# Kernel tuning notes

Hardware: AMD Instinct MI355X
Metric: run time of the kernel (lower is better)

Reference implementation:

```python
import jax, jax.numpy as jnp
import numpy as np

CHUNK = 256  # points per lax.map step; keeps [CHUNK, F] intermediates small


def _point_tri_sqdist(p_chunk, a, b, c):
    """Squared distance from each point to each triangle (Ericson closest-point).
    p_chunk: [C,3]; a,b,c: [F,3] -> returns [C,F]."""
    p = p_chunk[:, None, :]          # [C,1,3]
    a = a[None]; b = b[None]; c = c[None]  # [1,F,3]
    ab = b - a
    ac = c - a
    ap = p - a
    d1 = jnp.sum(ab * ap, -1)
    d2 = jnp.sum(ac * ap, -1)
    bp = p - b
    d3 = jnp.sum(ab * bp, -1)
    d4 = jnp.sum(ac * bp, -1)
    cp = p - c
    d5 = jnp.sum(ab * cp, -1)
    d6 = jnp.sum(ac * cp, -1)
    vc_ = d1 * d4 - d3 * d2
    vb_ = d5 * d2 - d1 * d6
    va_ = d3 * d6 - d5 * d4
    # safe-guarded edge / interior parameters
    den_ab = d1 - d3
    v_ab = d1 / jnp.where(den_ab != 0, den_ab, 1.0)
    den_ac = d2 - d6
    w_ac = d2 / jnp.where(den_ac != 0, den_ac, 1.0)
    den_bc = (d4 - d3) + (d5 - d6)
    w_bc = (d4 - d3) / jnp.where(den_bc != 0, den_bc, 1.0)
    den_in = va_ + vb_ + vc_
    inv = 1.0 / jnp.where(den_in != 0, den_in, 1.0)
    v_in = vb_ * inv
    w_in = vc_ * inv
    # candidate closest point; later writes take priority (vertex regions last)
    q = a + ab * v_in[..., None] + ac * w_in[..., None]                      # interior
    q = jnp.where(((va_ <= 0) & (d4 - d3 >= 0) & (d5 - d6 >= 0))[..., None],
                  b + (c - b) * w_bc[..., None], q)                          # edge bc
    q = jnp.where(((vb_ <= 0) & (d2 >= 0) & (d6 <= 0))[..., None],
                  a + ac * w_ac[..., None], q)                               # edge ac
    q = jnp.where(((vc_ <= 0) & (d1 >= 0) & (d3 <= 0))[..., None],
                  a + ab * v_ab[..., None], q)                               # edge ab
    q = jnp.where(((d6 >= 0) & (d5 <= d6))[..., None], c, q)                 # vertex c
    q = jnp.where(((d3 >= 0) & (d4 <= d3))[..., None], b, q)                 # vertex b
    q = jnp.where(((d1 <= 0) & (d2 <= 0))[..., None], a, q)                  # vertex a
    return jnp.sum((p - q) ** 2, -1)


def _mesh_sdf(verts, faces, points):
    va = verts[faces[:, 0]]
    vb = verts[faces[:, 1]]
    vc = verts[faces[:, 2]]

    def per_chunk(pc):
        d = _point_tri_sqdist(pc, va, vb, vc)   # [CHUNK, F]
        return jnp.min(d, axis=-1), jnp.argmin(d, axis=-1)

    P = points.shape[0]
    dists, assoc = jax.lax.map(per_chunk, points.reshape(P // CHUNK, CHUNK, 3))
    dist = dists.reshape(P)
    assoc = assoc.reshape(P).astype(jnp.int32)
    loss = jnp.sum(dist)
    return loss, dist, assoc


def setup_inputs() -> dict:
    key = jax.random.key(0)
    k1, k2, k3 = jax.random.split(key, 3)
    V, F, P = 8192, 16384, 16384
    verts = jax.random.uniform(k1, (V, 3), dtype=jnp.float32)
    faces = jax.random.randint(k2, (F, 3), 0, V, dtype=jnp.int32)
    points = jax.random.uniform(k3, (P, 3), dtype=jnp.float32)
    return {"verts": verts, "faces": faces, "points": points}


def reference(verts, faces, points):
    return _mesh_sdf(verts, faces, points)
```

## Files before the change

### kernel.cpp

```cpp
#include <hip/hip_runtime.h>
#include <math.h>


#define PTOT 16384
#define FTOT 16384
#define NBINS 4096
#define BLOCK 256
#define NCH 32
#define FCHUNK (FTOT / NCH)
#define QCAP 2048

#define WS_BEST    0
#define WS_SORTP   131072
#define WS_HISTP   393216
#define WS_HISTF   409600
#define WS_HISTFC  425984
#define WS_HINT    442368
#define WS_FA      507904
#define WS_FB      770048
#define WS_FC      1032192
#define WS_FSCAN   1294336
#define WS_FBAND   1556480
#define WS_FBOXC   1622016
#define WS_FBOXH   1884160
#define ZERO_BYTES (16384 + 16384)

__device__ __forceinline__ unsigned morton12(float x, float y, float z) {
    int ix = (int)(x * 16.0f); ix = ix < 0 ? 0 : (ix > 15 ? 15 : ix);
    int iy = (int)(y * 16.0f); iy = iy < 0 ? 0 : (iy > 15 ? 15 : iy);
    int iz = (int)(z * 16.0f); iz = iz < 0 ? 0 : (iz > 15 ? 15 : iz);
    unsigned code = 0;
#pragma unroll
    for (int k = 0; k < 4; ++k) {
        code |= (((unsigned)(ix >> k) & 1u) << (3 * k + 2))
              | (((unsigned)(iy >> k) & 1u) << (3 * k + 1))
              | (((unsigned)(iz >> k) & 1u) << (3 * k + 0));
    }
    return code;
}

__device__ __forceinline__ float exec_pair(
    float px, float py, float pz,
    float ax, float ay, float az,
    float bx, float by, float bz,
    float cx, float cy, float cz)
{
#pragma clang fp contract(off)
    const float abx = __fsub_rn(bx, ax), aby = __fsub_rn(by, ay), abz = __fsub_rn(bz, az);
    const float acx = __fsub_rn(cx, ax), acy = __fsub_rn(cy, ay), acz = __fsub_rn(cz, az);
    const float cbx = __fsub_rn(cx, bx), cby = __fsub_rn(cy, by), cbz = __fsub_rn(cz, bz);

    const float apx = __fsub_rn(px, ax), apy = __fsub_rn(py, ay), apz = __fsub_rn(pz, az);
    const float d1 = __fadd_rn(__fadd_rn(__fmul_rn(abx, apx), __fmul_rn(aby, apy)), __fmul_rn(abz, apz));
    const float d2 = __fadd_rn(__fadd_rn(__fmul_rn(acx, apx), __fmul_rn(acy, apy)), __fmul_rn(acz, apz));
    const float bpx = __fsub_rn(px, bx), bpy = __fsub_rn(py, by), bpz = __fsub_rn(pz, bz);
    const float d3 = __fadd_rn(__fadd_rn(__fmul_rn(abx, bpx), __fmul_rn(aby, bpy)), __fmul_rn(abz, bpz));
    const float d4 = __fadd_rn(__fadd_rn(__fmul_rn(acx, bpx), __fmul_rn(acy, bpy)), __fmul_rn(acz, bpz));
    const float cpx = __fsub_rn(px, cx), cpy = __fsub_rn(py, cy), cpz = __fsub_rn(pz, cz);
    const float d5 = __fadd_rn(__fadd_rn(__fmul_rn(abx, cpx), __fmul_rn(aby, cpy)), __fmul_rn(abz, cpz));
    const float d6 = __fadd_rn(__fadd_rn(__fmul_rn(acx, cpx), __fmul_rn(acy, cpy)), __fmul_rn(acz, cpz));

    const float vc_ = __fsub_rn(__fmul_rn(d1, d4), __fmul_rn(d3, d2));
    const float vb_ = __fsub_rn(__fmul_rn(d5, d2), __fmul_rn(d1, d6));
    const float va_ = __fsub_rn(__fmul_rn(d3, d6), __fmul_rn(d5, d4));

    const float den_ab = __fsub_rn(d1, d3);
    const float den_ac = __fsub_rn(d2, d6);
    const float t43    = __fsub_rn(d4, d3);
    const float t56    = __fsub_rn(d5, d6);
    const float den_bc = __fadd_rn(t43, t56);
    const float den_in = __fadd_rn(__fadd_rn(va_, vb_), vc_);

    const bool f_a  = (d1 <= 0.0f) && (d2 <= 0.0f);
    const bool f_b  = (d3 >= 0.0f) && (d4 <= d3);
    const bool f_c  = (d6 >= 0.0f) && (d5 <= d6);
    const bool f_ab = (vc_ <= 0.0f) && (d1 >= 0.0f) && (d3 <= 0.0f);
    const bool f_ac = (vb_ <= 0.0f) && (d2 >= 0.0f) && (d6 <= 0.0f);
    const bool f_bc = (va_ <= 0.0f) && (t43 >= 0.0f) && (t56 >= 0.0f);
    const bool vert = f_a || f_b || f_c;
    const bool e_ab = f_ab && !vert;
    const bool e_ac = f_ac && !vert && !f_ab;
    const bool e_bc = f_bc && !vert && !f_ab && !f_ac;
    const bool inte = !vert && !f_ab && !f_ac && !f_bc;

    const float num  = e_ab ? d1 : (e_ac ? d2 : (e_bc ? t43 : 1.0f));
    const float denr = e_ab ? den_ab : (e_ac ? den_ac : (e_bc ? den_bc : den_in));
    const float den  = (denr != 0.0f) ? denr : 1.0f;
    const float t    = __fdiv_rn(num, den);

    const float v_in = __fmul_rn(vb_, t);
    const float w_in = __fmul_rn(vc_, t);

    const float s1 = vert ? 0.0f : (inte ? v_in : t);
    const float s2 = inte ? w_in : 0.0f;
    const bool  sel_b = (!f_a && f_b) || e_bc;
    const bool  sel_c = !f_a && !f_b && f_c;
    const float e1x = e_ac ? acx : (e_bc ? cbx : abx);
    const float e1y = e_ac ? acy : (e_bc ? cby : aby);
    const float e1z = e_ac ? acz : (e_bc ? cbz : abz);
    const float bsx = sel_b ? bx : (sel_c ? cx : ax);
    const float bsy = sel_b ? by : (sel_c ? cy : ay);
    const float bsz = sel_b ? bz : (sel_c ? cz : az);
    const float qx = __fadd_rn(__fadd_rn(bsx, __fmul_rn(e1x, s1)), __fmul_rn(acx, s2));
    const float qy = __fadd_rn(__fadd_rn(bsy, __fmul_rn(e1y, s1)), __fmul_rn(acy, s2));
    const float qz = __fadd_rn(__fadd_rn(bsz, __fmul_rn(e1z, s1)), __fmul_rn(acz, s2));

    const float dxx = __fsub_rn(px, qx), dyy = __fsub_rn(py, qy), dzz = __fsub_rn(pz, qz);
    return __fadd_rn(__fadd_rn(__fmul_rn(dxx, dxx), __fmul_rn(dyy, dyy)), __fmul_rn(dzz, dzz));
}

__global__ __launch_bounds__(BLOCK) void hist_kernel(
    const float* __restrict__ verts, const int* __restrict__ faces,
    const float* __restrict__ points,
    unsigned* __restrict__ histP, unsigned* __restrict__ histF)
{
    const int b = blockIdx.x;
    if (b < 64) {
        const int p = b * BLOCK + threadIdx.x;
        atomicAdd(&histP[morton12(points[p*3], points[p*3+1], points[p*3+2])], 1u);
    } else {
        const int f = (b - 64) * BLOCK + threadIdx.x;
        const int i0 = faces[f*3+0], i1 = faces[f*3+1], i2 = faces[f*3+2];
        const float mx = (verts[i0*3+0] + verts[i1*3+0] + verts[i2*3+0]) * (1.0f/3.0f);
        const float my = (verts[i0*3+1] + verts[i1*3+1] + verts[i2*3+1]) * (1.0f/3.0f);
        const float mz = (verts[i0*3+2] + verts[i1*3+2] + verts[i2*3+2]) * (1.0f/3.0f);
        atomicAdd(&histF[morton12(mx, my, mz)], 1u);
    }
}

__global__ __launch_bounds__(256) void scan_kernel(
    unsigned* __restrict__ histP, unsigned* __restrict__ histF,
    unsigned* __restrict__ histFC)
{
    unsigned* h = (blockIdx.x == 0) ? histP : histF;
    __shared__ unsigned ps[256];
    const int t = threadIdx.x;
    unsigned local[16];
    unsigned run = 0;
#pragma unroll
    for (int i = 0; i < 16; ++i) { unsigned v = h[t*16+i]; local[i] = run; run += v; }
    ps[t] = run;
    __syncthreads();
    for (int off = 1; off < 256; off <<= 1) {
        unsigned v = (t >= off) ? ps[t - off] : 0u;
        __syncthreads();
        ps[t] += v;
        __syncthreads();
    }
    const unsigned base = (t == 0) ? 0u : ps[t-1];
#pragma unroll
    for (int i = 0; i < 16; ++i) {
        const unsigned off = base + local[i];
        h[t*16+i] = off;
        if (blockIdx.x == 1) histFC[t*16+i] = off;
    }
}

__global__ __launch_bounds__(BLOCK) void scatter_build_kernel(
    const float* __restrict__ verts, const int* __restrict__ faces,
    const float* __restrict__ points,
    unsigned* __restrict__ histP, unsigned* __restrict__ histF,
    uint4* __restrict__ sortP,
    float4* __restrict__ fA, float4* __restrict__ fB, float4* __restrict__ fC,
    float4* __restrict__ fScan, float* __restrict__ fBand,
    float4* __restrict__ fBoxC, float4* __restrict__ fBoxH)
{
    const int b = blockIdx.x;
    if (b < 64) {
        const int p = b * BLOCK + threadIdx.x;
        const float x = points[p*3], y = points[p*3+1], z = points[p*3+2];
        const unsigned pos = atomicAdd(&histP[morton12(x, y, z)], 1u);
        sortP[pos] = make_uint4(__float_as_uint(x), __float_as_uint(y),
                                __float_as_uint(z), (unsigned)p);
        return;
    }
    const int f = (b - 64) * BLOCK + threadIdx.x;
    const int i0 = faces[f*3+0], i1 = faces[f*3+1], i2 = faces[f*3+2];
    const float ax = verts[i0*3+0], ay = verts[i0*3+1], az = verts[i0*3+2];
    const float bx = verts[i1*3+0], by = verts[i1*3+1], bz = verts[i1*3+2];
    const float cx = verts[i2*3+0], cy = verts[i2*3+1], cz = verts[i2*3+2];
    const float mx = (ax+bx+cx) * (1.0f/3.0f);
    const float my = (ay+by+cy) * (1.0f/3.0f);
    const float mz = (az+bz+cz) * (1.0f/3.0f);
    const unsigned pos = atomicAdd(&histF[morton12(mx, my, mz)], 1u);

    fA[pos] = make_float4(ax, ay, az, __uint_as_float((unsigned)f));
    fB[pos] = make_float4(bx, by, bz, 0.0f);
    fC[pos] = make_float4(cx, cy, cz, 0.0f);

    const double abx = (double)bx-ax, aby = (double)by-ay, abz = (double)bz-az;
    const double acx = (double)cx-ax, acy = (double)cy-ay, acz = (double)cz-az;
    const double cbx = (double)cx-bx, cby = (double)cy-by, cbz = (double)cz-bz;
    const double nx = aby*acz - abz*acy;
    const double ny = abz*acx - abx*acz;
    const double nz = abx*acy - aby*acx;
    const double nn = nx*nx + ny*ny + nz*nz;
    const double e1 = sqrt(abx*abx + aby*aby + abz*abz);
    const double e2 = sqrt(acx*acx + acy*acy + acz*acz);
    const double e3 = sqrt(cbx*cbx + cby*cby + cbz*cbz);
    const double maxe = fmax(e1, fmax(e2, e3));
    const double mine = fmin(e1, fmin(e2, e3));
    const double mine2 = mine * mine;
    const double maxe2 = maxe * maxe;
    const double maxe3 = maxe2 * maxe;

    const bool exempt = !(nn > 1e-5 * maxe2) || !(mine2 > 5e-6 * maxe);

    float4 sc;
    float band, J;
    if (!exempt) {
        const double rin = 1.0 / sqrt(nn);
        sc.x = (float)(nx * rin);
        sc.y = (float)(ny * rin);
        sc.z = (float)(nz * rin);
        sc.w = (float)(-(nx*rin*ax + ny*rin*ay + nz*rin*az));
        band = (float)fmin(1e4, 3e-5 * maxe3 / nn + 2e-5);
        J    = (float)fmin(1e4, 1.2 * (6e-5 * maxe3 / nn
                                     + 5e-5 * maxe2 / mine2
                                     + 2.6e-6 * maxe / mine
                                     + 3.2e-3));
    } else {
        sc = make_float4(0.0f, 0.0f, 0.0f, 0.0f);
        band = 1e30f;
        J    = 1e30f;
    }
    fScan[pos] = sc;
    fBand[pos] = band;

    const double mnx = fmin((double)ax, fmin((double)bx, (double)cx));
    const double mxx = fmax((double)ax, fmax((double)bx, (double)cx));
    const double mny = fmin((double)ay, fmin((double)by, (double)cy));
    const double mxy = fmax((double)ay, fmax((double)by, (double)cy));
    const double mnz = fmin((double)az, fmin((double)bz, (double)cz));
    const double mxz = fmax((double)az, fmax((double)bz, (double)cz));
    const float ccx = (float)((mnx + mxx) * 0.5);
    const float ccy = (float)((mny + mxy) * 0.5);
    const float ccz = (float)((mnz + mxz) * 0.5);
    const float hx = (float)((mxx - mnx) * 0.5 * 1.0002 + 2e-5);
    const float hy = (float)((mxy - mny) * 0.5 * 1.0002 + 2e-5);
    const float hz = (float)((mxz - mnz) * 0.5 * 1.0002 + 2e-5);
    fBoxC[pos] = make_float4(ccx, ccy, ccz, hx);
    fBoxH[pos] = make_float4(hy, hz, J, 0.0f);
}

__global__ __launch_bounds__(BLOCK) void seed_kernel(
    const float* __restrict__ points,
    const unsigned* __restrict__ histFC,
    const float4* __restrict__ fA, const float4* __restrict__ fB,
    const float4* __restrict__ fC,
    unsigned long long* __restrict__ best, unsigned* __restrict__ hint)
{
    const int t = blockIdx.x * BLOCK + threadIdx.x;
    const int pid = t >> 1;
    const int s = t & 1;
    const float px = points[pid*3+0];
    const float py = points[pid*3+1];
    const float pz = points[pid*3+2];
    const unsigned code = morton12(px, py, pz);
    int w = (int)histFC[code] - 16;
    w = w < 0 ? 0 : (w > FTOT - 32 ? FTOT - 32 : w);

    unsigned long long pk = ~0ull;
    const int base = w + s * 16;
    for (int k = 0; k < 16; ++k) {
        const int i = base + k;
        const float4 A = fA[i], B = fB[i], C = fC[i];
        const float d = exec_pair(px, py, pz, A.x, A.y, A.z, B.x, B.y, B.z, C.x, C.y, C.z);
        const unsigned long long e =
            ((unsigned long long)__float_as_uint(d) << 32) | __float_as_uint(A.w);
        if (e < pk) pk = e;
    }
    const unsigned long long other = __shfl_xor(pk, 1, 64);
    if (other < pk) pk = other;
    if (s == 0) {
        best[pid] = pk;
        hint[pid] = __float_as_uint(sqrtf(__uint_as_float((unsigned)(pk >> 32))));
    }
}

__global__ __launch_bounds__(BLOCK) void sdf_main_kernel(
    const uint4* __restrict__ sortP,
    const float4* __restrict__ fScan, const float* __restrict__ fBand,
    const float4* __restrict__ fBoxC, const float4* __restrict__ fBoxH,
    const float4* __restrict__ fA, const float4* __restrict__ fB,
    const float4* __restrict__ fC,
    const unsigned* __restrict__ hint,
    unsigned long long* __restrict__ best)
{
    __shared__ float sPx[BLOCK], sPy[BLOCK], sPz[BLOCK];
    __shared__ unsigned sPid[BLOCK];
    __shared__ unsigned long long sBest[BLOCK];
    __shared__ unsigned sQ[QCAP];
    __shared__ unsigned sQcnt;

    const int tid = threadIdx.x;
    const uint4 sp = sortP[blockIdx.x * BLOCK + tid];
    const float px = __uint_as_float(sp.x);
    const float py = __uint_as_float(sp.y);
    const float pz = __uint_as_float(sp.z);
    const unsigned pid = sp.w;

    sPx[tid] = px; sPy[tid] = py; sPz[tid] = pz; sPid[tid] = pid;
    sBest[tid] = best[pid];
    if (tid == 0) sQcnt = 0;
    const float thr = __fmaf_rn(__uint_as_float(hint[pid]), 1.005f, 1e-3f);
    __syncthreads();

    const int fbase = (int)blockIdx.y * FCHUNK;

    for (int w0 = 0; w0 < FCHUNK; w0 += 64) {
        const int wb = fbase + w0;

#pragma unroll 4
        for (int k = 0; k < 64; ++k) {
            const float4 sc = fScan[wb + k];
            const float band = fBand[wb + k];
            const float4 BC = fBoxC[wb + k];
            const float4 BH = fBoxH[wb + k];
            const float pd = __fmaf_rn(sc.x, px, __fmaf_rn(sc.y, py, __fmaf_rn(sc.z, pz, sc.w)));
            const bool inband = !(fabsf(pd) > thr + band);
            const float ex = fmaxf(fabsf(px - BC.x) - BC.w, 0.0f);
            const float ey = fmaxf(fabsf(py - BC.y) - BH.x, 0.0f);
            const float ez = fmaxf(fabsf(pz - BC.z) - BH.y, 0.0f);
            const float lb2 = __fmaf_rn(ex, ex, __fmaf_rn(ey, ey, ez * ez));
            const float rhs = thr + BH.z;
            const bool inbox = !(lb2 > rhs * rhs);
            if (inband && inbox) {
                const unsigned idx = atomicAdd(&sQcnt, 1u);
                if (idx < QCAP) {
                    sQ[idx] = ((unsigned)tid << 16) | (unsigned)(wb + k);
                } else {
                    const int fi = wb + k;
                    const float4 A = fA[fi], B = fB[fi], C = fC[fi];
                    const float d = exec_pair(px, py, pz,
                        A.x, A.y, A.z, B.x, B.y, B.z, C.x, C.y, C.z);
                    const unsigned long long pk =
                        ((unsigned long long)__float_as_uint(d) << 32) | __float_as_uint(A.w);
                    atomicMin(&sBest[tid], pk);
                }
            }
        }

        __syncthreads();
        const unsigned n = (sQcnt < QCAP) ? sQcnt : QCAP;
        for (unsigned i = (unsigned)tid; i < n; i += BLOCK) {
            const unsigned e = sQ[i];
            const unsigned et = e >> 16;
            const int fi = (int)(e & 0xFFFFu);
            const float qx = sPx[et], qy = sPy[et], qz = sPz[et];
            const float4 A = fA[fi], B = fB[fi], C = fC[fi];
            const float d = exec_pair(qx, qy, qz,
                A.x, A.y, A.z, B.x, B.y, B.z, C.x, C.y, C.z);
            const unsigned long long pk =
                ((unsigned long long)__float_as_uint(d) << 32) | __float_as_uint(A.w);
            atomicMin(&sBest[et], pk);
        }
        __syncthreads();
        if (tid == 0) sQcnt = 0;
        __syncthreads();
    }

    atomicMin(&best[pid], sBest[tid]);
}

__global__ __launch_bounds__(BLOCK) void sdf_final_kernel(
    const unsigned long long* __restrict__ best, float* __restrict__ out)
{
    __shared__ float wsum[BLOCK / 64];
    const int p = blockIdx.x * BLOCK + threadIdx.x;
    const unsigned long long v = best[p];
    const float d = __uint_as_float((unsigned)(v >> 32));
    const int idx = (int)(unsigned)(v & 0xffffffffull);
    out[1 + p] = d;
    out[1 + PTOT + p] = (float)idx;

    float s = d;
    for (int off = 32; off > 0; off >>= 1) s += __shfl_down(s, off, 64);
    const int lane = threadIdx.x & 63;
    const int w = threadIdx.x >> 6;
    if (lane == 0) wsum[w] = s;
    __syncthreads();
    if (threadIdx.x == 0) {
        float tsum = 0.0f;
        for (int i = 0; i < BLOCK / 64; ++i) tsum += wsum[i];
        atomicAdd(&out[0], tsum);
    }
}

extern "C" void kernel_launch(void* const* d_in, const int* in_sizes, int n_in,
                              void* d_out, int out_size, void* d_ws, size_t ws_size,
                              hipStream_t stream) {
    const float* verts  = (const float*)d_in[0];
    const int*   faces  = (const int*)d_in[1];
    const float* points = (const float*)d_in[2];
    float* out = (float*)d_out;

    char* ws = (char*)d_ws;
    unsigned long long* best = (unsigned long long*)(ws + WS_BEST);
    uint4*    sortP   = (uint4*)(ws + WS_SORTP);
    unsigned* histP   = (unsigned*)(ws + WS_HISTP);
    unsigned* histF   = (unsigned*)(ws + WS_HISTF);
    unsigned* histFC  = (unsigned*)(ws + WS_HISTFC);
    unsigned* hint    = (unsigned*)(ws + WS_HINT);
    float4* fA    = (float4*)(ws + WS_FA);
    float4* fB    = (float4*)(ws + WS_FB);
    float4* fC    = (float4*)(ws + WS_FC);
    float4* fScan = (float4*)(ws + WS_FSCAN);
    float*  fBand = (float*)(ws + WS_FBAND);
    float4* fBoxC = (float4*)(ws + WS_FBOXC);
    float4* fBoxH = (float4*)(ws + WS_FBOXH);

    hipMemsetAsync(histP, 0, (size_t)ZERO_BYTES, stream);
    hipMemsetAsync(out, 0, sizeof(float), stream);

    hist_kernel<<<128, BLOCK, 0, stream>>>(verts, faces, points, histP, histF);
    scan_kernel<<<2, 256, 0, stream>>>(histP, histF, histFC);
    scatter_build_kernel<<<128, BLOCK, 0, stream>>>(verts, faces, points,
        histP, histF, sortP, fA, fB, fC, fScan, fBand, fBoxC, fBoxH);

    seed_kernel<<<2 * PTOT / BLOCK, BLOCK, 0, stream>>>(points, histFC,
        fA, fB, fC, best, hint);

    dim3 grid(PTOT / BLOCK, NCH);
    sdf_main_kernel<<<grid, BLOCK, 0, stream>>>(sortP,
        fScan, fBand, fBoxC, fBoxH, fA, fB, fC, hint, best);

    sdf_final_kernel<<<PTOT / BLOCK, BLOCK, 0, stream>>>(best, out);
}
```

Baseline: 309.4 us.

## Swap scan loop to face-per-lane with points broadcast from shared memory

```diff
diff --git a/kernel.cpp b/kernel.cpp
--- a/kernel.cpp
+++ b/kernel.cpp
@@ -8,7 +8,7 @@
 #define BLOCK 256
 #define NCH 32
 #define FCHUNK (FTOT / NCH)
-#define QCAP 2048
+#define QCAP 3072
 
 #define WS_BEST    0
 #define WS_SORTP   131072
@@ -287,56 +287,66 @@
     const unsigned* __restrict__ hint,
     unsigned long long* __restrict__ best)
 {
-    __shared__ float sPx[BLOCK], sPy[BLOCK], sPz[BLOCK];
-    __shared__ unsigned sPid[BLOCK];
+    __shared__ float4 sP[BLOCK];
     __shared__ unsigned long long sBest[BLOCK];
     __shared__ unsigned sQ[QCAP];
     __shared__ unsigned sQcnt;
 
     const int tid = threadIdx.x;
+    const unsigned lane = (unsigned)(tid & 63);
+    const int wave = tid >> 6;
+
     const uint4 sp = sortP[blockIdx.x * BLOCK + tid];
     const float px = __uint_as_float(sp.x);
     const float py = __uint_as_float(sp.y);
     const float pz = __uint_as_float(sp.z);
     const unsigned pid = sp.w;
 
-    sPx[tid] = px; sPy[tid] = py; sPz[tid] = pz; sPid[tid] = pid;
+    sP[tid] = make_float4(px, py, pz,
+                          __fmaf_rn(__uint_as_float(hint[pid]), 1.005f, 1e-3f));
     sBest[tid] = best[pid];
     if (tid == 0) sQcnt = 0;
-    const float thr = __fmaf_rn(__uint_as_float(hint[pid]), 1.005f, 1e-3f);
     __syncthreads();
 
     const int fbase = (int)blockIdx.y * FCHUNK;
 
-    for (int w0 = 0; w0 < FCHUNK; w0 += 64) {
-        const int wb = fbase + w0;
-
-#pragma unroll 4
-        for (int k = 0; k < 64; ++k) {
-            const float4 sc = fScan[wb + k];
-            const float band = fBand[wb + k];
-            const float4 BC = fBoxC[wb + k];
-            const float4 BH = fBoxH[wb + k];
-            const float pd = __fmaf_rn(sc.x, px, __fmaf_rn(sc.y, py, __fmaf_rn(sc.z, pz, sc.w)));
-            const bool inband = !(fabsf(pd) > thr + band);
-            const float ex = fmaxf(fabsf(px - BC.x) - BC.w, 0.0f);
-            const float ey = fmaxf(fabsf(py - BC.y) - BH.x, 0.0f);
-            const float ez = fmaxf(fabsf(pz - BC.z) - BH.y, 0.0f);
+    for (int r = 0; r < FCHUNK / (4 * 64); ++r) {
+        const int fi = fbase + (r * 4 + wave) * 64 + (int)lane;
+        const float4 sc = fScan[fi];
+        const float band = fBand[fi];
+        const float4 BC = fBoxC[fi];
+        const float4 BH = fBoxH[fi];
+
+        for (int p = 0; p < BLOCK; ++p) {
+            const float4 P = sP[p];
+            const float pd = __fmaf_rn(sc.x, P.x, __fmaf_rn(sc.y, P.y, __fmaf_rn(sc.z, P.z, sc.w)));
+            const bool inband = !(fabsf(pd) > P.w + band);
+            const float ex = fmaxf(fabsf(P.x - BC.x) - BC.w, 0.0f);
+            const float ey = fmaxf(fabsf(P.y - BC.y) - BH.x, 0.0f);
+            const float ez = fmaxf(fabsf(P.z - BC.z) - BH.y, 0.0f);
             const float lb2 = __fmaf_rn(ex, ex, __fmaf_rn(ey, ey, ez * ez));
-            const float rhs = thr + BH.z;
-            const bool inbox = !(lb2 > rhs * rhs);
-            if (inband && inbox) {
-                const unsigned idx = atomicAdd(&sQcnt, 1u);
-                if (idx < QCAP) {
-                    sQ[idx] = ((unsigned)tid << 16) | (unsigned)(wb + k);
-                } else {
-                    const int fi = wb + k;
-                    const float4 A = fA[fi], B = fB[fi], C = fC[fi];
-                    const float d = exec_pair(px, py, pz,
-                        A.x, A.y, A.z, B.x, B.y, B.z, C.x, C.y, C.z);
-                    const unsigned long long pk =
-                        ((unsigned long long)__float_as_uint(d) << 32) | __float_as_uint(A.w);
-                    atomicMin(&sBest[tid], pk);
+            const float rhs = P.w + BH.z;
+            const bool cand = inband && !(lb2 > rhs * rhs);
+            const unsigned long long cb = __ballot(cand);
+            if (cb) {
+                const int leader = (int)__builtin_ctzll(cb);
+                unsigned basei = 0;
+                if ((int)lane == leader)
+                    basei = atomicAdd(&sQcnt, (unsigned)__popcll(cb));
+                basei = __shfl(basei, leader, 64);
+                if (cand) {
+                    const unsigned off = (unsigned)__popcll(cb & ((1ull << lane) - 1ull));
+                    const unsigned slot = basei + off;
+                    if (slot < QCAP) {
+                        sQ[slot] = ((unsigned)p << 16) | (unsigned)fi;
+                    } else {
+                        const float4 A = fA[fi], B = fB[fi], C = fC[fi];
+                        const float d = exec_pair(P.x, P.y, P.z,
+                            A.x, A.y, A.z, B.x, B.y, B.z, C.x, C.y, C.z);
+                        const unsigned long long pk =
+                            ((unsigned long long)__float_as_uint(d) << 32) | __float_as_uint(A.w);
+                        atomicMin(&sBest[p], pk);
+                    }
                 }
             }
         }
@@ -345,15 +355,15 @@
         const unsigned n = (sQcnt < QCAP) ? sQcnt : QCAP;
         for (unsigned i = (unsigned)tid; i < n; i += BLOCK) {
             const unsigned e = sQ[i];
-            const unsigned et = e >> 16;
-            const int fi = (int)(e & 0xFFFFu);
-            const float qx = sPx[et], qy = sPy[et], qz = sPz[et];
-            const float4 A = fA[fi], B = fB[fi], C = fC[fi];
-            const float d = exec_pair(qx, qy, qz,
+            const unsigned pl = e >> 16;
+            const int f2 = (int)(e & 0xFFFFu);
+            const float4 P = sP[pl];
+            const float4 A = fA[f2], B = fB[f2], C = fC[f2];
+            const float d = exec_pair(P.x, P.y, P.z,
                 A.x, A.y, A.z, B.x, B.y, B.z, C.x, C.y, C.z);
             const unsigned long long pk =
                 ((unsigned long long)__float_as_uint(d) << 32) | __float_as_uint(A.w);
-            atomicMin(&sBest[et], pk);
+            atomicMin(&sBest[pl], pk);
         }
         __syncthreads();
         if (tid == 0) sQcnt = 0;
```

Measured after the change: 419.6 us. +35.6%, slower.
